# Performance work log

Hardware: AMD Instinct MI355X
Metric: run time of the kernel (lower is better)

The kernel has to match this reference:

```python
import jax, jax.numpy as jnp
import numpy as np

B, M, S, A = 256, 256, 32, 33
NH, NOUT = 3, 100
F_IN = 2 * S + 2          # 66, GAT input features
ALPHA = 0.01              # leaky-relu slope
LN_EPS = 1e-5


def setup_inputs() -> dict:
    key = jax.random.key(0)
    ks = jax.random.split(key, 13)
    obs_dim = 5 * M + 2 + 2 * M * S
    obs = jax.random.normal(ks[0], (B, obs_dim), jnp.float32)
    adj = jax.random.randint(ks[1], (M, M), 0, 2).astype(jnp.int32)
    u_gumbel = jax.random.uniform(ks[2], (B, M, A), jnp.float32)
    W_gat = jax.random.normal(ks[3], (NH, F_IN, NOUT), jnp.float32) * 0.1
    a_gat = jax.random.normal(ks[4], (NH, 2 * NOUT), jnp.float32) * 0.1
    ln_w = jax.random.normal(ks[5], (NH * NOUT,), jnp.float32) * 0.5
    ln_b = jnp.zeros((NH * NOUT,), jnp.float32)
    W1 = jax.random.normal(ks[6], (3 * M + 2, 100), jnp.float32) * 0.05
    b1 = jax.random.normal(ks[7], (100,), jnp.float32) * 0.7
    d2_in = 100 + NH * M * NOUT
    W2 = jax.random.normal(ks[8], (d2_in, 128), jnp.float32) * 0.005
    b2 = jax.random.normal(ks[9], (128,), jnp.float32) * 0.7
    Wout = jax.random.normal(ks[10], (M, 128, A), jnp.float32) * 0.1
    bout = jax.random.normal(ks[11], (M, A), jnp.float32) * 0.7
    return dict(obs=obs, adj=adj, u_gumbel=u_gumbel, W_gat=W_gat, a_gat=a_gat,
                ln_w=ln_w, ln_b=ln_b, W1=W1, b1=b1, W2=W2, b2=b2,
                Wout=Wout, bout=bout)


def _actor_fwd(obs, u_gumbel, W_gat, a_gat, ln_w, ln_b, W1, b1, W2, b2, Wout, bout, adj):
    # --- split obs per Actor.forward slicing ---
    server_state = obs[:, :3 * M + 2]                       # [B, 3m+2]
    mcs_res = obs[:, 3 * M + 2:4 * M + 2].reshape(B, M, 1)
    mcs_ins = obs[:, 4 * M + 2:5 * M + 2].reshape(B, M, 1)
    base = 5 * M + 2
    resp = obs[:, base:base + M * S].reshape(B, M, S)
    insp = obs[:, base + M * S:].reshape(B, M, S)
    feat = jnp.concatenate([mcs_res, mcs_ins, resp, insp], axis=-1)  # [B,M,2s+2]

    # --- GAT layer (eval mode: dropouts are identity) ---
    Wh = jnp.einsum('bmf,hfo->hbmo', feat, W_gat)           # [H,B,M,O]
    # e[b,i,j] = leakyrelu(a1 . Wh_i + a2 . Wh_j)  (same math as the
    # original O(N^2,2f) repeat/cat, expressed without materializing it)
    e1 = jnp.einsum('hbmo,ho->hbm', Wh, a_gat[:, :NOUT])
    e2 = jnp.einsum('hbmo,ho->hbm', Wh, a_gat[:, NOUT:])
    e = jax.nn.leaky_relu(e1[..., :, None] + e2[..., None, :], ALPHA)  # [H,B,M,M]
    e = jnp.where(adj > 0, e, jnp.float32(-9e15))
    att = jax.nn.softmax(e, axis=-2)                        # torch softmax(dim=1)
    h_prime = jax.nn.elu(jnp.einsum('hbij,hbjo->hbio', att, Wh))
    feats = jnp.moveaxis(h_prime, 0, 2).reshape(B, M, NH * NOUT)  # head concat
    mu = jnp.mean(feats, axis=-1, keepdims=True)
    var = jnp.var(feats, axis=-1, keepdims=True)
    gat_out = (feats - mu) * jax.lax.rsqrt(var + LN_EPS) * ln_w + ln_b
    gat_out = jax.nn.elu(gat_out)                           # GAT.forward elu_
    mcs_gat = gat_out.reshape(B, -1)                        # [B, 3*m*100]

    # --- dense heads ---
    server_feat = jax.nn.relu(jax.nn.elu(server_state @ W1 + b1))
    hidden = jax.nn.relu(jax.nn.elu(
        jnp.concatenate([server_feat, mcs_gat], axis=-1) @ W2 + b2))  # [B,128]

    # per-mcs heads, vectorized: logits[b,m,a]
    logits = jnp.tanh(jax.nn.elu(jnp.einsum('bh,mha->bma', hidden, Wout) + bout))

    # gumbel-softmax (tau=1, hard=True, straight-through)
    u = jnp.clip(u_gumbel, 1e-10, 1.0 - 1e-10)
    g = -jnp.log(-jnp.log(u))
    y_soft = jax.nn.softmax(logits + g, axis=-1)
    y_hard = jax.nn.one_hot(jnp.argmax(y_soft, axis=-1), A, dtype=y_soft.dtype)
    actions = y_hard + y_soft - jax.lax.stop_gradient(y_soft)
    return actions.reshape(B, M * A)


def reference(obs, adj, u_gumbel, W_gat, a_gat, ln_w, ln_b, W1, b1, W2, b2, Wout, bout):
    return _actor_fwd(obs, u_gumbel, W_gat, a_gat, ln_w, ln_b, W1, b1, W2, b2, Wout, bout, adj)
```

## Files before the change

kernel.cpp:

```cpp
#include <hip/hip_runtime.h>
#include <math.h>

constexpr int B    = 256;
constexpr int M    = 256;
constexpr int A    = 33;
constexpr int NH   = 3;
constexpr int NO   = 100;
constexpr int FIN  = 66;
constexpr int OBSD = 17666;
constexpr int D1   = 770;
constexpr int D2G  = 76800;

__device__ __forceinline__ float lrelu(float x) { return x > 0.f ? x : 0.01f * x; }
__device__ __forceinline__ float eluf(float x)  { return x > 0.f ? x : expm1f(x); }

__global__ __launch_bounds__(256) void k_adjmask(const int* __restrict__ adj,
                                                 unsigned* __restrict__ adjm) {
  int w = blockIdx.x * 256 + threadIdx.x;
  if (w >= M * 8) return;
  int i = w >> 3, wd = w & 7;
  const int* row = adj + i * M + wd * 32;
  unsigned mval = 0;
  #pragma unroll
  for (int bit = 0; bit < 32; ++bit) mval |= (row[bit] > 0 ? 1u : 0u) << bit;
  adjm[w] = mval;
}

__global__ __launch_bounds__(256) void k_wh(const float* __restrict__ obs,
                                            const float* __restrict__ Wg,
                                            const float* __restrict__ ag,
                                            const unsigned* __restrict__ adjm,
                                            float* __restrict__ Wh,
                                            float* __restrict__ e1,
                                            float* __restrict__ e2,
                                            float* __restrict__ cmax,
                                            float* __restrict__ csum) {
  int b = blockIdx.x, h = blockIdx.y;
  int t = threadIdx.x;
  int to = t >> 4;
  int tm = t & 15;
  __shared__ float smem_w[66 * 104 + 32];
  __shared__ float featT[66 * 132];
  __shared__ float a1s[128], a2s[128];
  __shared__ float e1a[256], e2a[256];
  __shared__ unsigned ams[M * 8];
  const float* ob = obs + (size_t)b * OBSD;

  for (int idx = t; idx < 66 * 104 + 32; idx += 256) {
    float v = 0.f;
    if (idx < 66 * 104) {
      int f = idx / 104, o = idx % 104;
      if (o < NO) v = Wg[((size_t)h * FIN + f) * NO + o];
    }
    smem_w[idx] = v;
  }
  if (t < 128) {
    a1s[t] = (t < NO) ? ag[h * 200 + t] : 0.f;
    a2s[t] = (t < NO) ? ag[h * 200 + NO + t] : 0.f;
  }
  for (int w = t; w < M * 8; w += 256) ams[w] = adjm[w];

  size_t basee = ((size_t)h * B + b) * M;

  for (int tile = 0; tile < 2; ++tile) {
    int m0 = tile * 128;
    if (t < 128)       featT[t]               = ob[770  + m0 + t];
    else               featT[132 + (t - 128)] = ob[1026 + m0 + (t - 128)];
    for (int idx = t; idx < 128 * 32; idx += 256) {
      int m = idx >> 5, s = idx & 31;
      featT[(2  + s) * 132 + m] = ob[1282 + (size_t)(m0 + m) * 32 + s];
      featT[(34 + s) * 132 + m] = ob[9474 + (size_t)(m0 + m) * 32 + s];
    }
    __syncthreads();

    float acc[8][8];
    #pragma unroll
    for (int q = 0; q < 8; ++q)
      #pragma unroll
      for (int p = 0; p < 8; ++p) acc[q][p] = 0.f;

    for (int f = 0; f < 66; ++f) {
      const float* fr = featT + f * 132 + tm * 8;
      const float* wr = smem_w + f * 104 + to * 8;
      float4 fa = *(const float4*)fr;
      float4 fb = *(const float4*)(fr + 4);
      float4 wa = *(const float4*)wr;
      float4 wb = *(const float4*)(wr + 4);
      float fm[8] = {fa.x, fa.y, fa.z, fa.w, fb.x, fb.y, fb.z, fb.w};
      float wv[8] = {wa.x, wa.y, wa.z, wa.w, wb.x, wb.y, wb.z, wb.w};
      #pragma unroll
      for (int q = 0; q < 8; ++q)
        #pragma unroll
        for (int p = 0; p < 8; ++p) acc[q][p] += fm[q] * wv[p];
    }
    __syncthreads();

    float* e1p = featT;
    float* e2p = featT + 128 * 18;
    #pragma unroll
    for (int q = 0; q < 8; ++q) {
      float p1 = 0.f, p2 = 0.f;
      #pragma unroll
      for (int p = 0; p < 8; ++p) {
        float av = acc[q][p];
        p1 += av * a1s[to * 8 + p];
        p2 += av * a2s[to * 8 + p];
      }
      e1p[(tm * 8 + q) * 18 + to] = p1;
      e2p[(tm * 8 + q) * 18 + to] = p2;
    }

    #pragma unroll
    for (int q = 0; q < 8; ++q) {
      int m = m0 + tm * 8 + q;
      float* wp = Wh + (basee + m) * NO + to * 8;
      if (to <= 12) *(float4*)wp       = make_float4(acc[q][0], acc[q][1], acc[q][2], acc[q][3]);
      if (to <= 11) *(float4*)(wp + 4) = make_float4(acc[q][4], acc[q][5], acc[q][6], acc[q][7]);
    }
    __syncthreads();

    if (t < 128) {
      float s1 = 0.f, s2 = 0.f;
      #pragma unroll
      for (int u = 0; u < 16; ++u) {
        s1 += e1p[t * 18 + u];
        s2 += e2p[t * 18 + u];
      }
      e1[basee + m0 + t] = s1;
      e2[basee + m0 + t] = s2;
      e1a[m0 + t] = s1;
      e2a[m0 + t] = s2;
    }
    __syncthreads();
  }

  {
    float e2j = e2a[t];
    int jw = t >> 5;
    unsigned jb = 1u << (t & 31);
    float mx = -INFINITY;
    for (int i = 0; i < M; ++i) {
      float v = (ams[i * 8 + jw] & jb) ? lrelu(e1a[i] + e2j) : -9e15f;
      mx = fmaxf(mx, v);
    }
    float sm = 0.f;
    for (int i = 0; i < M; ++i) {
      float v = (ams[i * 8 + jw] & jb) ? lrelu(e1a[i] + e2j) : -9e15f;
      sm += expf(v - mx);
    }
    cmax[basee + t] = mx;
    csum[basee + t] = sm;
  }
}

__global__ __launch_bounds__(256) void k_attn(const float* __restrict__ Wh,
                                              const float* __restrict__ e1,
                                              const float* __restrict__ e2,
                                              const float* __restrict__ cmax,
                                              const float* __restrict__ csum,
                                              const unsigned* __restrict__ adjm,
                                              float* __restrict__ feats) {
  int b = blockIdx.x, h = blockIdx.y, ih = blockIdx.z;
  int t = threadIdx.x;
  int to = t & 15, ti = t >> 4;
  int i0 = ih * 128;
  __shared__ float WhC[32 * 128];
  __shared__ float attT[32 * 132];
  __shared__ float e1s[128];
  __shared__ float e2s[256], cms[256], csr[256];
  size_t base = ((size_t)h * B + b) * M;

  if (t < 128) e1s[t] = e1[base + i0 + t];
  e2s[t] = e2[base + t];
  cms[t] = cmax[base + t];
  csr[t] = 1.0f / csum[base + t];

  float acc[8][8];
  #pragma unroll
  for (int q = 0; q < 8; ++q)
    #pragma unroll
    for (int p = 0; p < 8; ++p) acc[q][p] = 0.f;

  const float* WhG = Wh + base * NO;
  int jp = t >> 3;
  int il = (t & 7) * 16;

  for (int c = 0; c < 8; ++c) {
    __syncthreads();
    for (int idx = t; idx < 32 * 128; idx += 256) {
      int r = idx >> 7, o = idx & 127;
      WhC[idx] = (o < NO) ? WhG[(size_t)(c * 32 + r) * NO + o] : 0.f;
    }
    {
      int jg = c * 32 + jp;
      float e2j = e2s[jg], cmj = cms[jg], rsj = csr[jg];
      unsigned wbit = 1u << jp;
      const unsigned* aw = adjm + (size_t)(i0 + il) * 8 + c;
      const float* ep = e1s + il;
      float* ap = attT + jp * 132 + il;
      #pragma unroll
      for (int r = 0; r < 16; ++r) {
        float v = (aw[r * 8] & wbit) ? lrelu(ep[r] + e2j) : -9e15f;
        ap[r] = expf(v - cmj) * rsj;
      }
    }
    __syncthreads();
    for (int j = 0; j < 32; ++j) {
      const float4* a4 = (const float4*)(attT + j * 132 + ti * 8);
      float4 aa = a4[0], ab = a4[1];
      float4 wa = *(const float4*)(WhC + j * 128 + to * 4);
      float4 wb = *(const float4*)(WhC + j * 128 + 64 + to * 4);
      float av[8] = {aa.x, aa.y, aa.z, aa.w, ab.x, ab.y, ab.z, ab.w};
      float wv[8] = {wa.x, wa.y, wa.z, wa.w, wb.x, wb.y, wb.z, wb.w};
      #pragma unroll
      for (int q = 0; q < 8; ++q)
        #pragma unroll
        for (int p = 0; p < 8; ++p) acc[q][p] += av[q] * wv[p];
    }
  }

  #pragma unroll
  for (int q = 0; q < 8; ++q) {
    int i = i0 + ti * 8 + q;
    float* fp = feats + ((size_t)b * M + i) * 300 + h * NO;
    *(float4*)(fp + to * 4) =
        make_float4(eluf(acc[q][0]), eluf(acc[q][1]), eluf(acc[q][2]), eluf(acc[q][3]));
    if (to < 9)
      *(float4*)(fp + 64 + to * 4) =
          make_float4(eluf(acc[q][4]), eluf(acc[q][5]), eluf(acc[q][6]), eluf(acc[q][7]));
  }
}

__global__ __launch_bounds__(256) void k_lnstats(const float* __restrict__ g,
                                                 float* __restrict__ mu_out,
                                                 float* __restrict__ rs_out) {
  int gid = blockIdx.x * 256 + threadIdx.x;
  int wid = gid >> 6, lane = gid & 63;
  const float* row = g + (size_t)wid * 300;
  float v[5];
  float s = 0.f;
  #pragma unroll
  for (int j = 0; j < 5; ++j) {
    int i = j * 64 + lane;
    v[j] = (i < 300) ? row[i] : 0.f;
    s += v[j];
  }
  #pragma unroll
  for (int d = 1; d < 64; d <<= 1) s += __shfl_xor(s, d);
  float mu = s * (1.f / 300.f);
  float ss = 0.f;
  #pragma unroll
  for (int j = 0; j < 5; ++j) {
    int i = j * 64 + lane;
    float dd = (i < 300) ? (v[j] - mu) : 0.f;
    ss += dd * dd;
  }
  #pragma unroll
  for (int d = 1; d < 64; d <<= 1) ss += __shfl_xor(ss, d);
  if (lane == 0) {
    mu_out[wid] = mu;
    rs_out[wid] = 1.0f / sqrtf(ss * (1.f / 300.f) + 1e-5f);
  }
}

__global__ __launch_bounds__(256) void k_sf(const float* __restrict__ obs,
                                            const float* __restrict__ W1,
                                            const float* __restrict__ b1,
                                            float* __restrict__ sf) {
  int b = blockIdx.x, t = threadIdx.x;
  int k = t & 127, fc = t >> 7;
  __shared__ float ss[D1];
  __shared__ float red[256];
  const float* ob = obs + (size_t)b * OBSD;
  for (int i = t; i < D1; i += 256) ss[i] = ob[i];
  __syncthreads();
  float acc = 0.f;
  if (k < NO) {
    int f0 = fc * 385;
    #pragma unroll 8
    for (int f = f0; f < f0 + 385; ++f) acc += ss[f] * W1[(size_t)f * NO + k];
  }
  red[t] = acc;
  __syncthreads();
  if (t < 128 && k < NO) {
    float v = red[t] + red[t + 128] + b1[k];
    sf[b * NO + k] = fmaxf(eluf(v), 0.f);
  }
}

__global__ __launch_bounds__(256) void k_gemm2(const float* __restrict__ gat,
                                               const float* __restrict__ mu,
                                               const float* __restrict__ rs,
                                               const float* __restrict__ lw,
                                               const float* __restrict__ lb,
                                               const float* __restrict__ W2,
                                               float* __restrict__ pre) {
  int lid = blockIdx.y * 16 + blockIdx.x;
  int xg = lid & 7, rr0 = lid >> 3;
  int dc = xg * 8 + (rr0 >> 4);
  int bt = rr0 & 15;
  int t = threadIdx.x;
  int k = t & 127, g2 = t >> 7;
  __shared__ float gt[16 * 124];
  int b0 = bt * 16, d0 = dc * 1200;
  float acc[8];
  #pragma unroll
  for (int r = 0; r < 8; ++r) acc[r] = 0.f;
  for (int ds0 = 0; ds0 < 1200; ds0 += 120) {
    int dsg = d0 + ds0;
    __syncthreads();
    for (int idx = t; idx < 16 * 120; idx += 256) {
      int rr = idx / 120, cc = idx - rr * 120;
      int gidx = dsg + cc;
      int brow = b0 + rr;
      int mrow = gidx / 300;
      int d    = gidx - mrow * 300;
      int lrow = brow * M + mrow;
      float x = gat[(size_t)brow * D2G + gidx];
      float val = (x - mu[lrow]) * rs[lrow] * lw[d] + lb[d];
      gt[rr * 124 + cc] = eluf(val);
    }
    __syncthreads();
    const float* w2p = W2 + (size_t)(100 + dsg) * 128 + k;
    for (int c4 = 0; c4 < 30; ++c4) {
      float w0  = w2p[(size_t)(c4 * 4 + 0) * 128];
      float w1  = w2p[(size_t)(c4 * 4 + 1) * 128];
      float w2v = w2p[(size_t)(c4 * 4 + 2) * 128];
      float w3  = w2p[(size_t)(c4 * 4 + 3) * 128];
      #pragma unroll
      for (int r = 0; r < 8; ++r) {
        float4 gv = *(const float4*)(gt + (g2 * 8 + r) * 124 + c4 * 4);
        acc[r] += gv.x * w0 + gv.y * w1 + gv.z * w2v + gv.w * w3;
      }
    }
  }
  #pragma unroll
  for (int r = 0; r < 8; ++r)
    pre[((size_t)dc * B + b0 + g2 * 8 + r) * 128 + k] = acc[r];
}

__global__ __launch_bounds__(256) void k_hid(const float* __restrict__ pre,
                                             const float* __restrict__ sf,
                                             const float* __restrict__ W2,
                                             const float* __restrict__ b2,
                                             float* __restrict__ hid,
                                             float* __restrict__ hidT) {
  int b = blockIdx.x, t = threadIdx.x;
  int k = t & 127, p = t >> 7;
  __shared__ float red[256];
  float s = 0.f;
  const float* sfb = sf + b * NO;
  #pragma unroll 4
  for (int dc = p * 32; dc < p * 32 + 32; ++dc)
    s += pre[((size_t)dc * B + b) * 128 + k];
  #pragma unroll 4
  for (int f = p * 50; f < p * 50 + 50; ++f)
    s += sfb[f] * W2[(size_t)f * 128 + k];
  red[t] = s;
  __syncthreads();
  if (t < 128) {
    float v = red[t] + red[t + 128] + b2[k];
    v = fmaxf(eluf(v), 0.f);
    hid[(size_t)b * 128 + k] = v;
    hidT[(size_t)k * B + b]  = v;
  }
}

__global__ __launch_bounds__(256) void k_out(const float* __restrict__ hidT,
                                             const float* __restrict__ Wout,
                                             const float* __restrict__ bout,
                                             const float* __restrict__ ug,
                                             float* __restrict__ out) {
  int m = blockIdx.x, b = threadIdx.x;
  __shared__ float wo[128 * 36];
  for (int idx = b; idx < 128 * 36; idx += 256) {
    int kk = idx / 36, a = idx % 36;
    wo[idx] = (a < A) ? Wout[(size_t)m * 128 * A + kk * A + a] : 0.f;
  }
  __syncthreads();
  float l[36];
  #pragma unroll
  for (int a = 0; a < 36; ++a) l[a] = (a < A) ? bout[m * A + a] : 0.f;
  for (int kk = 0; kk < 128; ++kk) {
    float hv = hidT[(size_t)kk * B + b];
    const float4* w4 = (const float4*)(wo + kk * 36);
    #pragma unroll
    for (int q = 0; q < 9; ++q) {
      float4 wv = w4[q];
      l[4*q+0] += hv * wv.x;
      l[4*q+1] += hv * wv.y;
      l[4*q+2] += hv * wv.z;
      l[4*q+3] += hv * wv.w;
    }
  }
  const float* ugp = ug + ((size_t)b * M + m) * A;
  float mx = -INFINITY;
  int amx = 0;
  #pragma unroll
  for (int a = 0; a < A; ++a) {
    float th = tanhf(eluf(l[a]));
    float u = ugp[a];
    u = fminf(fmaxf(u, 1e-10f), 1.0f - 1e-10f);
    float gb = -logf(-logf(u));
    float z = th + gb;
    l[a] = z;
    if (z > mx) { mx = z; amx = a; }
  }
  float sm = 0.f;
  #pragma unroll
  for (int a = 0; a < A; ++a) { float e = expf(l[a] - mx); l[a] = e; sm += e; }
  float* op = out + ((size_t)b * M + m) * A;
  #pragma unroll
  for (int a = 0; a < A; ++a) {
    float ys = l[a] / sm;
    float yh = (a == amx) ? 1.0f : 0.0f;
    op[a] = (yh + ys) - ys;
  }
}

extern "C" void kernel_launch(void* const* d_in, const int* in_sizes, int n_in,
                              void* d_out, int out_size, void* d_ws, size_t ws_size,
                              hipStream_t stream) {
  const float* obs  = (const float*)d_in[0];
  const int*   adj  = (const int*)  d_in[1];
  const float* ug   = (const float*)d_in[2];
  const float* Wg   = (const float*)d_in[3];
  const float* ag   = (const float*)d_in[4];
  const float* lw   = (const float*)d_in[5];
  const float* lb   = (const float*)d_in[6];
  const float* W1   = (const float*)d_in[7];
  const float* b1   = (const float*)d_in[8];
  const float* W2   = (const float*)d_in[9];
  const float* b2   = (const float*)d_in[10];
  const float* Wout = (const float*)d_in[11];
  const float* bout = (const float*)d_in[12];
  float* out = (float*)d_out;

  float* ws = (float*)d_ws;
  size_t off = 0;
  float* Wh    = ws + off; off += (size_t)NH * B * M * NO;
  float* feats = ws + off; off += (size_t)B * M * 300;
  float* e1    = ws + off; off += (size_t)NH * B * M;
  float* e2    = ws + off; off += (size_t)NH * B * M;
  float* cmx   = ws + off; off += (size_t)NH * B * M;
  float* csm   = ws + off; off += (size_t)NH * B * M;
  float* sf    = ws + off; off += (size_t)B * NO;
  float* pre   = ws + off; off += (size_t)64 * B * 128;
  float* hid   = ws + off; off += (size_t)B * 128;
  float* hidT  = ws + off; off += (size_t)B * 128;
  float* muA   = ws + off; off += (size_t)B * M;
  float* rsA   = ws + off; off += (size_t)B * M;
  unsigned* adjm = (unsigned*)(ws + off);

  k_adjmask <<<dim3(8),         256, 0, stream>>>(adj, adjm);
  k_wh      <<<dim3(B, NH),     256, 0, stream>>>(obs, Wg, ag, adjm, Wh, e1, e2, cmx, csm);
  k_attn    <<<dim3(B, NH, 2),  256, 0, stream>>>(Wh, e1, e2, cmx, csm, adjm, feats);
  k_lnstats <<<dim3(B * M / 4), 256, 0, stream>>>(feats, muA, rsA);
  k_sf      <<<dim3(B),         256, 0, stream>>>(obs, W1, b1, sf);
  k_gemm2   <<<dim3(16, 64),    256, 0, stream>>>(feats, muA, rsA, lw, lb, W2, pre);
  k_hid     <<<dim3(B),         256, 0, stream>>>(pre, sf, W2, b2, hid, hidT);
  k_out     <<<dim3(M),         256, 0, stream>>>(hidT, Wout, bout, ug, out);
}
```

Baseline: 781.2 us.

## Fuse server-feature MLP into hidden kernel and fix LDS access strides

```diff
diff --git a/kernel.cpp b/kernel.cpp
--- a/kernel.cpp
+++ b/kernel.cpp
@@ -80,10 +80,10 @@
       for (int p = 0; p < 8; ++p) acc[q][p] = 0.f;
 
     for (int f = 0; f < 66; ++f) {
-      const float* fr = featT + f * 132 + tm * 8;
+      const float* fr = featT + f * 132;
       const float* wr = smem_w + f * 104 + to * 8;
-      float4 fa = *(const float4*)fr;
-      float4 fb = *(const float4*)(fr + 4);
+      float4 fa = *(const float4*)(fr + tm * 4);
+      float4 fb = *(const float4*)(fr + 64 + tm * 4);
       float4 wa = *(const float4*)wr;
       float4 wb = *(const float4*)(wr + 4);
       float fm[8] = {fa.x, fa.y, fa.z, fa.w, fb.x, fb.y, fb.z, fb.w};
@@ -99,6 +99,7 @@
     float* e2p = featT + 128 * 18;
     #pragma unroll
     for (int q = 0; q < 8; ++q) {
+      int ml = (q < 4) ? (tm * 4 + q) : (64 + tm * 4 + q - 4);
       float p1 = 0.f, p2 = 0.f;
       #pragma unroll
       for (int p = 0; p < 8; ++p) {
@@ -106,13 +107,14 @@
         p1 += av * a1s[to * 8 + p];
         p2 += av * a2s[to * 8 + p];
       }
-      e1p[(tm * 8 + q) * 18 + to] = p1;
-      e2p[(tm * 8 + q) * 18 + to] = p2;
+      e1p[ml * 18 + to] = p1;
+      e2p[ml * 18 + to] = p2;
     }
 
     #pragma unroll
     for (int q = 0; q < 8; ++q) {
-      int m = m0 + tm * 8 + q;
+      int ml = (q < 4) ? (tm * 4 + q) : (64 + tm * 4 + q - 4);
+      int m = m0 + ml;
       float* wp = Wh + (basee + m) * NO + to * 8;
       if (to <= 12) *(float4*)wp       = make_float4(acc[q][0], acc[q][1], acc[q][2], acc[q][3]);
       if (to <= 11) *(float4*)(wp + 4) = make_float4(acc[q][4], acc[q][5], acc[q][6], acc[q][7]);
@@ -139,11 +141,13 @@
     int jw = t >> 5;
     unsigned jb = 1u << (t & 31);
     float mx = -INFINITY;
+    #pragma unroll 8
     for (int i = 0; i < M; ++i) {
       float v = (ams[i * 8 + jw] & jb) ? lrelu(e1a[i] + e2j) : -9e15f;
       mx = fmaxf(mx, v);
     }
     float sm = 0.f;
+    #pragma unroll 8
     for (int i = 0; i < M; ++i) {
       float v = (ams[i * 8 + jw] & jb) ? lrelu(e1a[i] + e2j) : -9e15f;
       sm += expf(v - mx);
@@ -183,7 +187,7 @@
 
   const float* WhG = Wh + base * NO;
   int jp = t >> 3;
-  int il = (t & 7) * 16;
+  int ib = t & 7;
 
   for (int c = 0; c < 8; ++c) {
     __syncthreads();
@@ -195,13 +199,13 @@
       int jg = c * 32 + jp;
       float e2j = e2s[jg], cmj = cms[jg], rsj = csr[jg];
       unsigned wbit = 1u << jp;
-      const unsigned* aw = adjm + (size_t)(i0 + il) * 8 + c;
-      const float* ep = e1s + il;
-      float* ap = attT + jp * 132 + il;
-      #pragma unroll
-      for (int r = 0; r < 16; ++r) {
-        float v = (aw[r * 8] & wbit) ? lrelu(ep[r] + e2j) : -9e15f;
-        ap[r] = expf(v - cmj) * rsj;
+      const unsigned* aw = adjm + (size_t)(i0 + ib) * 8 + c;
+      const float* ep = e1s + ib;
+      float* ap = attT + jp * 132 + ib;
+      #pragma unroll
+      for (int rr = 0; rr < 16; ++rr) {
+        float v = (aw[rr * 64] & wbit) ? lrelu(ep[rr * 8] + e2j) : -9e15f;
+        ap[rr * 8] = expf(v - cmj) * rsj;
       }
     }
     __syncthreads();
@@ -263,31 +267,6 @@
   }
 }
 
-__global__ __launch_bounds__(256) void k_sf(const float* __restrict__ obs,
-                                            const float* __restrict__ W1,
-                                            const float* __restrict__ b1,
-                                            float* __restrict__ sf) {
-  int b = blockIdx.x, t = threadIdx.x;
-  int k = t & 127, fc = t >> 7;
-  __shared__ float ss[D1];
-  __shared__ float red[256];
-  const float* ob = obs + (size_t)b * OBSD;
-  for (int i = t; i < D1; i += 256) ss[i] = ob[i];
-  __syncthreads();
-  float acc = 0.f;
-  if (k < NO) {
-    int f0 = fc * 385;
-    #pragma unroll 8
-    for (int f = f0; f < f0 + 385; ++f) acc += ss[f] * W1[(size_t)f * NO + k];
-  }
-  red[t] = acc;
-  __syncthreads();
-  if (t < 128 && k < NO) {
-    float v = red[t] + red[t + 128] + b1[k];
-    sf[b * NO + k] = fmaxf(eluf(v), 0.f);
-  }
-}
-
 __global__ __launch_bounds__(256) void k_gemm2(const float* __restrict__ gat,
                                                const float* __restrict__ mu,
                                                const float* __restrict__ rs,
@@ -295,10 +274,7 @@
                                                const float* __restrict__ lb,
                                                const float* __restrict__ W2,
                                                float* __restrict__ pre) {
-  int lid = blockIdx.y * 16 + blockIdx.x;
-  int xg = lid & 7, rr0 = lid >> 3;
-  int dc = xg * 8 + (rr0 >> 4);
-  int bt = rr0 & 15;
+  int bt = blockIdx.x, dc = blockIdx.y;
   int t = threadIdx.x;
   int k = t & 127, g2 = t >> 7;
   __shared__ float gt[16 * 124];
@@ -340,22 +316,42 @@
 }
 
 __global__ __launch_bounds__(256) void k_hid(const float* __restrict__ pre,
-                                             const float* __restrict__ sf,
+                                             const float* __restrict__ obs,
+                                             const float* __restrict__ W1,
+                                             const float* __restrict__ b1,
                                              const float* __restrict__ W2,
                                              const float* __restrict__ b2,
                                              float* __restrict__ hid,
                                              float* __restrict__ hidT) {
   int b = blockIdx.x, t = threadIdx.x;
   int k = t & 127, p = t >> 7;
+  __shared__ float ssrv[D1];
+  __shared__ float sfs[128];
   __shared__ float red[256];
+  const float* ob = obs + (size_t)b * OBSD;
+  for (int i = t; i < D1; i += 256) ssrv[i] = ob[i];
+  __syncthreads();
+  float acc = 0.f;
+  if (k < NO) {
+    int f0 = p * 385;
+    #pragma unroll 8
+    for (int f = f0; f < f0 + 385; ++f) acc += ssrv[f] * W1[(size_t)f * NO + k];
+  }
+  red[t] = acc;
+  __syncthreads();
+  if (t < 128 && k < NO) {
+    float v = red[t] + red[t + 128] + b1[k];
+    sfs[k] = fmaxf(eluf(v), 0.f);
+  }
+  __syncthreads();
   float s = 0.f;
-  const float* sfb = sf + b * NO;
   #pragma unroll 4
   for (int dc = p * 32; dc < p * 32 + 32; ++dc)
     s += pre[((size_t)dc * B + b) * 128 + k];
   #pragma unroll 4
   for (int f = p * 50; f < p * 50 + 50; ++f)
-    s += sfb[f] * W2[(size_t)f * 128 + k];
+    s += sfs[f] * W2[(size_t)f * 128 + k];
+  __syncthreads();
   red[t] = s;
   __syncthreads();
   if (t < 128) {
@@ -444,7 +440,6 @@
   float* e2    = ws + off; off += (size_t)NH * B * M;
   float* cmx   = ws + off; off += (size_t)NH * B * M;
   float* csm   = ws + off; off += (size_t)NH * B * M;
-  float* sf    = ws + off; off += (size_t)B * NO;
   float* pre   = ws + off; off += (size_t)64 * B * 128;
   float* hid   = ws + off; off += (size_t)B * 128;
   float* hidT  = ws + off; off += (size_t)B * 128;
@@ -456,8 +451,7 @@
   k_wh      <<<dim3(B, NH),     256, 0, stream>>>(obs, Wg, ag, adjm, Wh, e1, e2, cmx, csm);
   k_attn    <<<dim3(B, NH, 2),  256, 0, stream>>>(Wh, e1, e2, cmx, csm, adjm, feats);
   k_lnstats <<<dim3(B * M / 4), 256, 0, stream>>>(feats, muA, rsA);
-  k_sf      <<<dim3(B),         256, 0, stream>>>(obs, W1, b1, sf);
   k_gemm2   <<<dim3(16, 64),    256, 0, stream>>>(feats, muA, rsA, lw, lb, W2, pre);
-  k_hid     <<<dim3(B),         256, 0, stream>>>(pre, sf, W2, b2, hid, hidT);
+  k_hid     <<<dim3(B),         256, 0, stream>>>(pre, obs, W1, b1, W2, b2, hid, hidT);
   k_out     <<<dim3(M),         256, 0, stream>>>(hidT, Wout, bout, ug, out);
 }
```

New measurement: 777.0 us. About the same (-0.5%).
